# Kernel optimization log

Hardware: AMD Instinct MI355X
Metric: run time of the kernel (lower is better)

The kernel has to match this reference:

```python
import jax, jax.numpy as jnp
import numpy as np

RATIO = 4


def setup_inputs() -> dict:
    key = jax.random.key(0)
    ks = jax.random.split(key, 6)
    b, c, hw = 8, 64, 256
    n = (hw // RATIO) ** 2  # 4096
    return {
        "x": jax.random.normal(ks[0], (b, c, hw, hw), dtype=jnp.float32),
        "weight": jax.random.normal(ks[1], (n, n), dtype=jnp.float32) * 0.01,
        "pih_w": jax.random.normal(ks[2], (c, c, 3, 3), dtype=jnp.float32) * 0.05,
        "pih_b": jax.random.normal(ks[3], (c,), dtype=jnp.float32) * 0.05,
        "up_w": jax.random.normal(ks[4], (c, c, 4, 4), dtype=jnp.float32) * 0.05,
        "up_b": jax.random.normal(ks[5], (c,), dtype=jnp.float32) * 0.05,
    }


def reference(x, weight, pih_w, pih_b, up_w, up_b):
    b, c, h, w = x.shape
    identity = x
    # MaxPool2d(ratio)
    xp = jax.lax.reduce_window(x, -jnp.inf, jax.lax.max,
                               (1, 1, RATIO, RATIO), (1, 1, RATIO, RATIO), 'VALID')
    # 3x3 conv, pad 1
    x_pih = jax.lax.conv_general_dilated(
        xp, pih_w, window_strides=(1, 1), padding='SAME',
        dimension_numbers=('NCHW', 'OIHW', 'NCHW')) + pih_b[None, :, None, None]
    x_pih = jax.nn.relu(x_pih).reshape(b, c, -1)  # [b, c, N]
    # F.normalize(p=2, dim=2)
    nrm = jnp.sqrt(jnp.sum(x_pih * x_pih, axis=2, keepdims=True))
    nx = x_pih / jnp.maximum(nrm, 1e-12)
    # channel-channel affinity [b, c, c]
    A = jnp.einsum('bcn,bdn->bcd', nx, nx)
    # vectorized D^{-1/2}, replacing per-batch torch.diag loop
    d = 1.0 / jnp.sqrt(jnp.sum(A, axis=2) + 1e-8)  # [b, c]
    d = jnp.where(jnp.isfinite(d), d, 0.0)
    L = jnp.eye(c, dtype=x.dtype)[None] - d[:, :, None] * A * d[:, None, :]
    # diffusion: L @ x_flat @ W
    xf = xp.reshape(b, c, -1)  # [b, c, N]
    out = jnp.einsum('bcd,bdn->bcn', L, xf)
    out = jnp.einsum('bcn,nm->bcm', out, weight)
    hp, wp = h // RATIO, w // RATIO
    out = out.reshape(b, c, hp, wp)
    # ConvTranspose2d(k=4, s=4): each pixel expands to a 4x4 block
    up = jnp.einsum('bchw,coij->bohiwj', out, up_w).reshape(b, c, h, w)
    up = up + up_b[None, :, None, None]
    return jax.nn.relu(up + identity)
```

## Files before the change

kernel.cpp:

```cpp
#include <hip/hip_runtime.h>

#define NB 8
#define NC 64
#define HW 256
#define HP 64
#define NN 4096

typedef unsigned short u16;
typedef unsigned int u32;
typedef __attribute__((ext_vector_type(8))) short s16x8;
typedef __attribute__((ext_vector_type(8))) unsigned short u16x8;
typedef __attribute__((ext_vector_type(4))) unsigned short u16x4;
typedef __attribute__((ext_vector_type(4))) float f32x4;

__device__ __forceinline__ u16 f2bf(float f) {
    unsigned u = __float_as_uint(f);
    return (u16)((u + 0x7fffu + ((u >> 16) & 1u)) >> 16);
}
__device__ __forceinline__ float bf2f(u16 v) {
    return __uint_as_float(((unsigned)v) << 16);
}

#define GLOAD16(gsrc, ldst) \
    __builtin_amdgcn_global_load_lds((const __attribute__((address_space(1))) unsigned int*)(gsrc), \
                                     (__attribute__((address_space(3))) unsigned int*)(ldst), 16, 0, 0)

__global__ __launch_bounds__(256) void maxpool_nhwc_k(const float* __restrict__ x,
                                                      u16* __restrict__ xpc) {
    __shared__ u16 tile[64 * 66];
    int bid = blockIdx.x;
    int b = bid >> 6, y = bid & 63;
    int t = threadIdx.x;
    int cl  = t >> 3;
    int seg = t & 7;
#pragma unroll
    for (int pass = 0; pass < 2; ++pass) {
        int c = pass * 32 + cl;
        const float* p = x + ((long)(b * 64 + c) * 256 + y * 4) * 256 + seg * 32;
        float m[8];
#pragma unroll
        for (int i = 0; i < 8; ++i) m[i] = -3.4e38f;
#pragma unroll
        for (int r = 0; r < 4; ++r)
#pragma unroll
            for (int i = 0; i < 8; ++i) {
                float4 v = *(const float4*)(p + r * 256 + i * 4);
                m[i] = fmaxf(m[i], fmaxf(fmaxf(v.x, v.y), fmaxf(v.z, v.w)));
            }
#pragma unroll
        for (int i = 0; i < 8; ++i) tile[c * 66 + seg * 8 + i] = f2bf(m[i]);
    }
    __syncthreads();
    int xo = t >> 2, cp = t & 3;
    u16x8 o0, o1;
#pragma unroll
    for (int e = 0; e < 8; ++e) o0[e] = tile[(cp * 16 + e) * 66 + xo];
#pragma unroll
    for (int e = 0; e < 8; ++e) o1[e] = tile[(cp * 16 + 8 + e) * 66 + xo];
    u16* dst = xpc + ((long)(b * 4096 + y * 64 + xo)) * 64 + cp * 16;
    *(u16x8*)dst = o0;
    *(u16x8*)(dst + 8) = o1;
}

__global__ __launch_bounds__(256) void transW_k(const float* __restrict__ W,
                                                u16* __restrict__ WTb) {
    __shared__ alignas(16) u16 tile[128 * 128];
    int k0 = (blockIdx.x >> 5) * 128;
    int n0 = (blockIdx.x & 31) * 128;
    int t = threadIdx.x;
    int nq = t & 31;
#pragma unroll
    for (int p = 0; p < 4; ++p) {
        int kq = (t >> 5) + p * 8;
        float4 v[4];
#pragma unroll
        for (int j = 0; j < 4; ++j)
            v[j] = *(const float4*)&W[(long)(k0 + kq * 4 + j) * 4096 + n0 + nq * 4];
#pragma unroll
        for (int jn = 0; jn < 4; ++jn) {
            int n = nq * 4 + jn;
            u16x4 c4;
            c4[0] = f2bf(((const float*)&v[0])[jn]);
            c4[1] = f2bf(((const float*)&v[1])[jn]);
            c4[2] = f2bf(((const float*)&v[2])[jn]);
            c4[3] = f2bf(((const float*)&v[3])[jn]);
            *(u16x4*)((char*)tile + n * 256 + ((kq * 8) ^ ((n & 15) << 4))) = c4;
        }
    }
    __syncthreads();
#pragma unroll
    for (int q = 0; q < 8; ++q) {
        int chunk = t + q * 256;
        int n = chunk >> 4, seg = chunk & 15;
        u16x8 o = *(const u16x8*)((const char*)tile + n * 256 +
                                  ((seg * 16) ^ ((n & 15) << 4)));
        *(u16x8*)&WTb[(long)(n0 + n) * 4096 + k0 + seg * 8] = o;
    }
}

__global__ __launch_bounds__(256) void prep_k(const float* __restrict__ uw,
                                              const float* __restrict__ pw,
                                              u16* __restrict__ Wb,
                                              u16* __restrict__ Bpack) {
    int bid = blockIdx.x;
    int t = threadIdx.x;
    if (bid < 256) {
        int idx = bid * 256 + t;
        int c = idx & 63;
        int n = idx >> 6;
        int o = n >> 4, i = (n >> 2) & 3, j = n & 3;
        Wb[idx] = f2bf(uw[((c * 64 + o) * 4 + i) * 4 + j]);
    } else {
        int idx = (bid - 256) * 256 + t;
        if (idx >= 36864) return;
        int e = idx & 7, l = (idx >> 3) & 63, nf = (idx >> 9) & 3, s = idx >> 11;
        int ch = s & 1, kd = s >> 1;
        int dy = kd / 3, dx = kd % 3;
        int o  = nf * 16 + (l & 15);
        int ci = ch * 32 + (l >> 4) * 8 + e;
        Bpack[idx] = f2bf(pw[((o * 64 + ci) * 3 + dy) * 3 + dx]);
    }
}

__global__ __launch_bounds__(256) void convgram_k(const u16* __restrict__ xpc,
                                                  const u16* __restrict__ Bpack,
                                                  const float* __restrict__ pb,
                                                  float* __restrict__ G) {
    __shared__ alignas(16) u16 ldsIn[3 * 66 * 64];
    __shared__ alignas(16) u16 ldsX[64 * 64];
    int bid = blockIdx.x;
    int b = bid >> 6, y = bid & 63;
    int t = threadIdx.x;
    int w = t >> 6, l = t & 63;
    int lr = l & 15, ksub = l >> 4;

    if (t < 48) {
        int r = t >> 4, q = t & 15;
        int off = r * 8448 + (q < 8 ? q * 16 : 8320 + (q - 8) * 16);
        *(u16x8*)((char*)ldsIn + off) = (u16x8){0, 0, 0, 0, 0, 0, 0, 0};
    }
#pragma unroll
    for (int i = 0; i < 6; ++i) {
        int r  = i >> 1;
        int ya = y - 1 + r;
        int wro = (i & 1) * 4096 + t * 16;
        int dst = r * 8448 + 128 + wro;
        if (ya >= 0 && ya < 64) {
            int xsl = 1 + (wro >> 7);
            int srcoff = (wro & ~127) | ((wro & 127) ^ ((xsl & 7) << 4));
            GLOAD16((const char*)xpc + (long)(b * 64 + ya) * 8192 + srcoff,
                    (char*)ldsIn + dst);
        } else {
            *(u16x8*)((char*)ldsIn + dst) = (u16x8){0, 0, 0, 0, 0, 0, 0, 0};
        }
    }
    __syncthreads();

    f32x4 acc[4];
#pragma unroll
    for (int mf = 0; mf < 4; ++mf) acc[mf] = (f32x4){0.f, 0.f, 0.f, 0.f};

#pragma unroll
    for (int kd = 0; kd < 9; ++kd) {
        int dy = kd / 3, dx = kd % 3;
#pragma unroll
        for (int ch = 0; ch < 2; ++ch) {
            int s = kd * 2 + ch;
            s16x8 bfrag = *(const s16x8*)(Bpack + ((s * 4 + w) * 64 + l) * 8);
#pragma unroll
            for (int mf = 0; mf < 4; ++mf) {
                int xsl  = mf * 16 + lr + dx;
                int coff = (ch * 64 + ksub * 16) ^ ((xsl & 7) << 4);
                s16x8 af = *(const s16x8*)((const char*)ldsIn +
                                           dy * 8448 + xsl * 128 + coff);
                acc[mf] = __builtin_amdgcn_mfma_f32_16x16x32_bf16(
                    af, bfrag, acc[mf], 0, 0, 0);
            }
        }
    }
    int o = w * 16 + lr;
    float bias = pb[o];
#pragma unroll
    for (int mf = 0; mf < 4; ++mf)
#pragma unroll
        for (int rp = 0; rp < 2; ++rp) {
            u16 lo = f2bf(fmaxf(acc[mf][rp * 2]     + bias, 0.f));
            u16 hi = f2bf(fmaxf(acc[mf][rp * 2 + 1] + bias, 0.f));
            int nb   = (mf * 16 + ksub * 4 + rp * 2) * 2;
            int boff = nb ^ ((o & 7) << 4);
            *(u32*)((char*)ldsX + o * 128 + boff) = (u32)lo | ((u32)hi << 16);
        }
    __syncthreads();

    f32x4 g[4];
#pragma unroll
    for (int nf = 0; nf < 4; ++nf) g[nf] = (f32x4){0.f, 0.f, 0.f, 0.f};
#pragma unroll
    for (int kk = 0; kk < 2; ++kk) {
        int kb = kk * 64 + ksub * 16;
        int arow = w * 16 + lr;
        s16x8 af = *(const s16x8*)((const char*)ldsX + arow * 128 +
                                   (kb ^ ((arow & 7) << 4)));
#pragma unroll
        for (int nf = 0; nf < 4; ++nf) {
            int brow = nf * 16 + lr;
            s16x8 bf = *(const s16x8*)((const char*)ldsX + brow * 128 +
                                       (kb ^ ((brow & 7) << 4)));
            g[nf] = __builtin_amdgcn_mfma_f32_16x16x32_bf16(af, bf, g[nf], 0, 0, 0);
        }
    }
    float* Gb = G + b * 4096;
#pragma unroll
    for (int nf = 0; nf < 4; ++nf)
#pragma unroll
        for (int r = 0; r < 4; ++r)
            atomicAdd(&Gb[(w * 16 + ksub * 4 + r) * 64 + nf * 16 + lr], g[nf][r]);
}

__global__ __launch_bounds__(256) void diffuse_mfma_k(const float* __restrict__ G,
                                                      const u16* __restrict__ xpc,
                                                      u16* __restrict__ Ab16) {
    __shared__ alignas(16) u16 lds[128 * 64];
    __shared__ alignas(16) u16 ldsL[64 * 64];
    __shared__ float nrm[64], dvv[64];
    int n0 = blockIdx.x * 128;
    int b  = blockIdx.y;
    int t = threadIdx.x;
    int w = t >> 6, l = t & 63;
    int lr = l & 15, ksub = l >> 4;

#pragma unroll
    for (int i = 0; i < 4; ++i) {
        int d = i * 4096 + t * 16;
        int row = d >> 7, off = d & 127;
        GLOAD16((const char*)xpc + ((long)(b * 4096 + n0 + row)) * 128 +
                (off ^ ((row & 7) << 4)),
                (char*)lds + d);
    }

    const float* Gb = G + b * 4096;
    if (t < 64) nrm[t] = fmaxf(sqrtf(Gb[t * 64 + t]), 1e-12f);
    __syncthreads();
    if (t < 64) {
        float nc = nrm[t];
        float rs = 0.f;
        for (int d = 0; d < 64; ++d) rs += Gb[t * 64 + d] / (nc * nrm[d]);
        float dd = 1.0f / sqrtf(rs + 1e-8f);
        if (!(dd <= 3.0e38f)) dd = 0.0f;
        dvv[t] = dd;
    }
    __syncthreads();
    {
        int c = t >> 2;
        int dbase = (t & 3) * 16;
        float nc = nrm[c], dc = dvv[c];
#pragma unroll
        for (int dp2 = 0; dp2 < 8; ++dp2) {
            int d0 = dbase + dp2 * 2;
            float A0 = Gb[c * 64 + d0]     / (nc * nrm[d0]);
            float A1 = Gb[c * 64 + d0 + 1] / (nc * nrm[d0 + 1]);
            float v0 = ((c == d0)     ? 1.f : 0.f) - dc * A0 * dvv[d0];
            float v1 = ((c == d0 + 1) ? 1.f : 0.f) - dc * A1 * dvv[d0 + 1];
            int o = c * 64 + (d0 ^ ((c & 7) << 3));
            *(u32*)&ldsL[o] = (u32)f2bf(v0) | ((u32)f2bf(v1) << 16);
        }
    }
    __syncthreads();

    f32x4 acc[4][2];
#pragma unroll
    for (int mf = 0; mf < 4; ++mf)
#pragma unroll
        for (int nq = 0; nq < 2; ++nq) acc[mf][nq] = (f32x4){0.f, 0.f, 0.f, 0.f};

#pragma unroll
    for (int kk = 0; kk < 2; ++kk) {
        s16x8 bfr[2];
#pragma unroll
        for (int nq = 0; nq < 2; ++nq) {
            int brow = w * 32 + nq * 16 + lr;
            bfr[nq] = *(const s16x8*)((const char*)lds + brow * 128 +
                                      ((kk * 64 + ksub * 16) ^ ((brow & 7) << 4)));
        }
#pragma unroll
        for (int mf = 0; mf < 4; ++mf) {
            int arow = mf * 16 + lr;
            s16x8 af = *(const s16x8*)((const char*)ldsL + arow * 128 +
                                       ((kk * 64 + ksub * 16) ^ ((arow & 7) << 4)));
#pragma unroll
            for (int nq = 0; nq < 2; ++nq)
                acc[mf][nq] = __builtin_amdgcn_mfma_f32_16x16x32_bf16(
                    af, bfr[nq], acc[mf][nq], 0, 0, 0);
        }
    }
#pragma unroll
    for (int mf = 0; mf < 4; ++mf)
#pragma unroll
        for (int nq = 0; nq < 2; ++nq)
#pragma unroll
            for (int r = 0; r < 4; ++r)
                Ab16[((long)(b * 64 + mf * 16 + (l >> 4) * 4 + r)) * 4096 +
                     n0 + w * 32 + nq * 16 + lr] = f2bf(acc[mf][nq][r]);
}

#define KSPLIT 4
#define KSLICE 1024
__global__ __launch_bounds__(256) void gemm_mfma_k(const u16* __restrict__ A,
                                                   const u16* __restrict__ WT,
                                                   u16* __restrict__ Cp) {
    __shared__ alignas(16) u16 ldsA[8192];
    __shared__ alignas(16) u16 ldsB[8192];
    int bid = blockIdx.x;
    int swz = (bid & 7) * 64 + (bid >> 3);
    int m0 = (swz & 3) * 128;
    int n0 = ((swz >> 2) & 31) * 128;
    int z  = swz >> 7;
    int t = threadIdx.x;
    int w = t >> 6, l = t & 63;
    int wr = w >> 1, wc = w & 1;
    int lr = l & 15;
    int lk = (l >> 4) << 4;

    f32x4 acc[4][4];
#pragma unroll
    for (int mf = 0; mf < 4; ++mf)
#pragma unroll
        for (int nf = 0; nf < 4; ++nf) acc[mf][nf] = (f32x4){0.f, 0.f, 0.f, 0.f};

    const char* Ab = (const char*)(A  + (long)m0 * 4096 + z * KSLICE);
    const char* Bb = (const char*)(WT + (long)n0 * 4096 + z * KSLICE);

    for (int k0 = 0; k0 < KSLICE; k0 += 64) {
        __syncthreads();
#pragma unroll
        for (int i = 0; i < 4; ++i) {
            int d   = i * 4096 + t * 16;
            int row = d >> 7;
            int off = d & 127;
            int sk  = off ^ ((row & 7) << 4);
            GLOAD16(Ab + (long)row * 8192 + k0 * 2 + sk, (char*)ldsA + d);
            GLOAD16(Bb + (long)row * 8192 + k0 * 2 + sk, (char*)ldsB + d);
        }
        __syncthreads();
#pragma unroll
        for (int kk = 0; kk < 2; ++kk) {
            s16x8 af[4], bf[4];
#pragma unroll
            for (int f = 0; f < 4; ++f) {
                int ar = wr * 64 + f * 16 + lr;
                af[f] = *(const s16x8*)((const char*)ldsA + ar * 128 +
                                        ((kk * 64 + lk) ^ ((ar & 7) << 4)));
                int br = wc * 64 + f * 16 + lr;
                bf[f] = *(const s16x8*)((const char*)ldsB + br * 128 +
                                        ((kk * 64 + lk) ^ ((br & 7) << 4)));
            }
#pragma unroll
            for (int mf = 0; mf < 4; ++mf)
#pragma unroll
                for (int nf = 0; nf < 4; ++nf)
                    acc[mf][nf] = __builtin_amdgcn_mfma_f32_16x16x32_bf16(
                        af[mf], bf[nf], acc[mf][nf], 0, 0, 0);
        }
    }
    int tile = (swz & 3) * 32 + ((swz >> 2) & 31);
    u16 carr[64];
#pragma unroll
    for (int mf = 0; mf < 4; ++mf)
#pragma unroll
        for (int nf = 0; nf < 4; ++nf)
#pragma unroll
            for (int r = 0; r < 4; ++r)
                carr[mf * 16 + nf * 4 + r] = f2bf(acc[mf][nf][r]);
    u16* dp = Cp + ((long)(z * 128 + tile) * 256 + t) * 64;
#pragma unroll
    for (int v8 = 0; v8 < 8; ++v8)
        *(u16x8*)&dp[v8 * 8] = *(const u16x8*)&carr[v8 * 8];
}

__global__ __launch_bounds__(256) void convT_mfma_k(const u16* __restrict__ Cp,
                                                    const u16* __restrict__ Wb,
                                                    const float* __restrict__ ub,
                                                    const float* __restrict__ x,
                                                    float* __restrict__ out) {
    __shared__ alignas(16) char smem[34816];
    u16*   ldsA = (u16*)smem;
    u16*   ldsB = (u16*)(smem + 16384);
    float* ldsC = (float*)smem;
    int bid = blockIdx.x;
    int swzb = (bid & 7) * 256 + (bid >> 3);
    int mt = swzb >> 3;
    int nt = swzb & 7;
    int m0 = mt * 128;
    int n0 = nt * 128;
    int t = threadIdx.x;
    int w = t >> 6, l = t & 63;
    int wr = w >> 1, wc = w & 1;
    int lr = l & 15;
    int lkb = (l >> 4) << 4;

    const char* Bb = (const char*)(Wb + (long)n0 * 64);
#pragma unroll
    for (int i = 0; i < 4; ++i) {
        int d = i * 4096 + t * 16;
        int srcoff = (d & ~127) | ((d & 127) ^ (((d >> 7) & 7) << 4));
        GLOAD16(Bb + srcoff, (char*)ldsB + d);
    }

    {
        int b_   = mt >> 5;
        int wr_g = b_ & 1;
        int tile_g = (b_ >> 1) * 32 + (mt & 31);
        int tg = wr_g * 128 + (t & 127);
        int h  = t >> 7;
        int l_g = tg & 63, wc_g = (tg >> 6) & 1;
        int k4 = l_g >> 4, lr_g = l_g & 15;
        float s[32];
#pragma unroll
        for (int k = 0; k < 32; ++k) s[k] = 0.f;
        const u16* dpb = Cp + ((long)tile_g * 256 + tg) * 64 + h * 32;
#pragma unroll
        for (int z = 0; z < KSPLIT; ++z) {
            const u16* pz = dpb + (long)z * 2097152;
#pragma unroll
            for (int j = 0; j < 4; ++j) {
                u16x8 vv = *(const u16x8*)&pz[j * 8];
#pragma unroll
                for (int e = 0; e < 8; ++e) s[j * 8 + e] += bf2f(vv[e]);
            }
        }
#pragma unroll
        for (int j = 0; j < 4; ++j) {
            int v8 = h * 4 + j;
            int mf = v8 >> 1;
            int c0 = mf * 16 + k4 * 4;
#pragma unroll
            for (int q = 0; q < 2; ++q) {
                int nf  = (v8 & 1) * 2 + q;
                int pix = wc_g * 64 + nf * 16 + lr_g;
                int sw  = (pix & 7) << 4;
                int f   = j * 8 + q * 4;
                u32 w0 = (u32)f2bf(s[f + 0]) | ((u32)f2bf(s[f + 1]) << 16);
                u32 w1 = (u32)f2bf(s[f + 2]) | ((u32)f2bf(s[f + 3]) << 16);
                *(u32*)((char*)ldsA + pix * 128 + ((c0 * 2) ^ sw))     = w0;
                *(u32*)((char*)ldsA + pix * 128 + ((c0 * 2 + 4) ^ sw)) = w1;
            }
        }
    }
    __syncthreads();

    f32x4 acc[4][4];
#pragma unroll
    for (int mf = 0; mf < 4; ++mf)
#pragma unroll
        for (int nf = 0; nf < 4; ++nf) acc[mf][nf] = (f32x4){0.f, 0.f, 0.f, 0.f};

#pragma unroll
    for (int kk = 0; kk < 2; ++kk) {
        s16x8 af[4], bfg[4];
#pragma unroll
        for (int f = 0; f < 4; ++f) {
            int ar = wr * 64 + f * 16 + lr;
            af[f] = *(const s16x8*)((const char*)ldsA + ar * 128 +
                                    ((kk * 64 + lkb) ^ ((ar & 7) << 4)));
            int br = wc * 64 + f * 16 + lr;
            bfg[f] = *(const s16x8*)((const char*)ldsB + br * 128 +
                                     ((kk * 64 + lkb) ^ ((br & 7) << 4)));
        }
#pragma unroll
        for (int mf = 0; mf < 4; ++mf)
#pragma unroll
            for (int nf = 0; nf < 4; ++nf)
                acc[mf][nf] = __builtin_amdgcn_mfma_f32_16x16x32_bf16(
                    af[mf], bfg[nf], acc[mf][nf], 0, 0, 0);
    }
    __syncthreads();

#pragma unroll
    for (int nh = 0; nh < 2; ++nh) {
        if (nh) __syncthreads();
        if (wc == nh) {
#pragma unroll
            for (int mf = 0; mf < 4; ++mf)
#pragma unroll
                for (int nf = 0; nf < 4; ++nf)
#pragma unroll
                    for (int r = 0; r < 4; ++r) {
                        int row = wr * 64 + mf * 16 + (l >> 4) * 4 + r;
                        int col = nf * 16 + lr;
                        ldsC[row * 68 + (col ^ (((row >> 3) & 7) << 2))] =
                            acc[mf][nf][r];
                    }
        }
        __syncthreads();
#pragma unroll
        for (int q = 0; q < 2; ++q) {
            int idx = q * 256 + t;
            int ml = idx & 127;
            int oo = idx >> 7;
            int o  = nt * 8 + nh * 4 + oo;
            float bias = ub[o];
            int mg = m0 + ml;
            int b = mg >> 12, pix = mg & 4095;
            int h2 = pix >> 6, ww = pix & 63;
            long base = ((long)(b * 64 + o) * 256 + h2 * 4) * 256 + ww * 4;
#pragma unroll
            for (int i = 0; i < 4; ++i) {
                f32x4 cv = *(const f32x4*)&ldsC[ml * 68 +
                            ((oo * 16 + i * 4) ^ (((ml >> 3) & 7) << 2))];
                float4 xi = *(const float4*)&x[base + i * 256];
                float4 rr;
                rr.x = fmaxf(cv[0] + bias + xi.x, 0.f);
                rr.y = fmaxf(cv[1] + bias + xi.y, 0.f);
                rr.z = fmaxf(cv[2] + bias + xi.z, 0.f);
                rr.w = fmaxf(cv[3] + bias + xi.w, 0.f);
                *(float4*)&out[base + i * 256] = rr;
            }
        }
    }
}

extern "C" void kernel_launch(void* const* d_in, const int* in_sizes, int n_in,
                              void* d_out, int out_size, void* d_ws, size_t ws_size,
                              hipStream_t stream) {
    const float* x      = (const float*)d_in[0];
    const float* weight = (const float*)d_in[1];
    const float* pih_w  = (const float*)d_in[2];
    const float* pih_b  = (const float*)d_in[3];
    const float* up_w   = (const float*)d_in[4];
    const float* up_b   = (const float*)d_in[5];
    float* out = (float*)d_out;
    float* ws  = (float*)d_ws;

    u16*   xpc   = (u16*)ws;
    u16*   Ab16  = (u16*)(ws + 3145728);
    float* G     = ws + 4194304;
    u16*   Wb    = (u16*)(ws + 4259840);
    u16*   WTb   = (u16*)(ws + 4325376);
    u16*   Cp    = (u16*)(ws + 12713984);
    u16*   Bpack = Cp + 2097152;

    hipMemsetAsync(G, 0, 32768 * sizeof(float), stream);
    maxpool_nhwc_k<<<512, 256, 0, stream>>>(x, xpc);
    transW_k      <<<1024, 256, 0, stream>>>(weight, WTb);
    prep_k        <<<400, 256, 0, stream>>>(up_w, pih_w, Wb, Bpack);
    convgram_k    <<<512, 256, 0, stream>>>(xpc, Bpack, pih_b, G);
    diffuse_mfma_k<<<dim3(32, 8), 256, 0, stream>>>(G, xpc, Ab16);
    gemm_mfma_k   <<<512, 256, 0, stream>>>(Ab16, WTb, Cp);
    convT_mfma_k  <<<2048, 256, 0, stream>>>(Cp, Wb, up_b, x, out);
}
```

Before: 163.2 us.

## Drop split-K in big GEMM, write transposed output directly; merge front prep kernels

The 512x4096x4096 GEMM moves from a 128x128 tile with 4-way split-K, which wrote bf16 partials and made the convT kernel sum them, to a 64x64 tile over the full K range. The output goes through LDS and is stored transposed in the pixel-major layout convT expects, so convT can load its A operand directly with global_load_lds. Separately, the maxpool, weight-transpose and param-prep kernels are merged into one launch. This removes the partial-sum traffic and two launches. The cost is smaller tiles with less operand reuse (each wave does 2x2 MFMAs per k-step) and a longer serial K loop per block.

```diff
diff --git a/kernel.cpp b/kernel.cpp
--- a/kernel.cpp
+++ b/kernel.cpp
@@ -25,100 +25,100 @@
     __builtin_amdgcn_global_load_lds((const __attribute__((address_space(1))) unsigned int*)(gsrc), \
                                      (__attribute__((address_space(3))) unsigned int*)(ldst), 16, 0, 0)
 
-__global__ __launch_bounds__(256) void maxpool_nhwc_k(const float* __restrict__ x,
-                                                      u16* __restrict__ xpc) {
-    __shared__ u16 tile[64 * 66];
-    int bid = blockIdx.x;
-    int b = bid >> 6, y = bid & 63;
-    int t = threadIdx.x;
-    int cl  = t >> 3;
-    int seg = t & 7;
-#pragma unroll
-    for (int pass = 0; pass < 2; ++pass) {
-        int c = pass * 32 + cl;
-        const float* p = x + ((long)(b * 64 + c) * 256 + y * 4) * 256 + seg * 32;
-        float m[8];
-#pragma unroll
-        for (int i = 0; i < 8; ++i) m[i] = -3.4e38f;
-#pragma unroll
-        for (int r = 0; r < 4; ++r)
-#pragma unroll
-            for (int i = 0; i < 8; ++i) {
-                float4 v = *(const float4*)(p + r * 256 + i * 4);
-                m[i] = fmaxf(m[i], fmaxf(fmaxf(v.x, v.y), fmaxf(v.z, v.w)));
-            }
-#pragma unroll
-        for (int i = 0; i < 8; ++i) tile[c * 66 + seg * 8 + i] = f2bf(m[i]);
-    }
-    __syncthreads();
-    int xo = t >> 2, cp = t & 3;
-    u16x8 o0, o1;
-#pragma unroll
-    for (int e = 0; e < 8; ++e) o0[e] = tile[(cp * 16 + e) * 66 + xo];
-#pragma unroll
-    for (int e = 0; e < 8; ++e) o1[e] = tile[(cp * 16 + 8 + e) * 66 + xo];
-    u16* dst = xpc + ((long)(b * 4096 + y * 64 + xo)) * 64 + cp * 16;
-    *(u16x8*)dst = o0;
-    *(u16x8*)(dst + 8) = o1;
-}
-
-__global__ __launch_bounds__(256) void transW_k(const float* __restrict__ W,
-                                                u16* __restrict__ WTb) {
-    __shared__ alignas(16) u16 tile[128 * 128];
-    int k0 = (blockIdx.x >> 5) * 128;
-    int n0 = (blockIdx.x & 31) * 128;
-    int t = threadIdx.x;
-    int nq = t & 31;
-#pragma unroll
-    for (int p = 0; p < 4; ++p) {
-        int kq = (t >> 5) + p * 8;
-        float4 v[4];
-#pragma unroll
-        for (int j = 0; j < 4; ++j)
-            v[j] = *(const float4*)&W[(long)(k0 + kq * 4 + j) * 4096 + n0 + nq * 4];
-#pragma unroll
-        for (int jn = 0; jn < 4; ++jn) {
-            int n = nq * 4 + jn;
-            u16x4 c4;
-            c4[0] = f2bf(((const float*)&v[0])[jn]);
-            c4[1] = f2bf(((const float*)&v[1])[jn]);
-            c4[2] = f2bf(((const float*)&v[2])[jn]);
-            c4[3] = f2bf(((const float*)&v[3])[jn]);
-            *(u16x4*)((char*)tile + n * 256 + ((kq * 8) ^ ((n & 15) << 4))) = c4;
-        }
-    }
-    __syncthreads();
-#pragma unroll
-    for (int q = 0; q < 8; ++q) {
-        int chunk = t + q * 256;
-        int n = chunk >> 4, seg = chunk & 15;
-        u16x8 o = *(const u16x8*)((const char*)tile + n * 256 +
-                                  ((seg * 16) ^ ((n & 15) << 4)));
-        *(u16x8*)&WTb[(long)(n0 + n) * 4096 + k0 + seg * 8] = o;
-    }
-}
-
-__global__ __launch_bounds__(256) void prep_k(const float* __restrict__ uw,
-                                              const float* __restrict__ pw,
-                                              u16* __restrict__ Wb,
-                                              u16* __restrict__ Bpack) {
+__global__ __launch_bounds__(256) void front_k(const float* __restrict__ x,
+                                               const float* __restrict__ W,
+                                               const float* __restrict__ uw,
+                                               const float* __restrict__ pw,
+                                               u16* __restrict__ xpc,
+                                               u16* __restrict__ WTb,
+                                               u16* __restrict__ Wb,
+                                               u16* __restrict__ Bpack) {
+    __shared__ alignas(16) char sm[32768];
     int bid = blockIdx.x;
     int t = threadIdx.x;
-    if (bid < 256) {
-        int idx = bid * 256 + t;
-        int c = idx & 63;
-        int n = idx >> 6;
-        int o = n >> 4, i = (n >> 2) & 3, j = n & 3;
-        Wb[idx] = f2bf(uw[((c * 64 + o) * 4 + i) * 4 + j]);
+    if (bid < 512) {
+        u16* tile = (u16*)sm;
+        int b = bid >> 6, y = bid & 63;
+        int cl  = t >> 3;
+        int seg = t & 7;
+#pragma unroll
+        for (int pass = 0; pass < 2; ++pass) {
+            int c = pass * 32 + cl;
+            const float* p = x + ((long)(b * 64 + c) * 256 + y * 4) * 256 + seg * 32;
+            float m[8];
+#pragma unroll
+            for (int i = 0; i < 8; ++i) m[i] = -3.4e38f;
+#pragma unroll
+            for (int r = 0; r < 4; ++r)
+#pragma unroll
+                for (int i = 0; i < 8; ++i) {
+                    float4 v = *(const float4*)(p + r * 256 + i * 4);
+                    m[i] = fmaxf(m[i], fmaxf(fmaxf(v.x, v.y), fmaxf(v.z, v.w)));
+                }
+#pragma unroll
+            for (int i = 0; i < 8; ++i) tile[c * 66 + seg * 8 + i] = f2bf(m[i]);
+        }
+        __syncthreads();
+        int xo = t >> 2, cp = t & 3;
+        u16x8 o0, o1;
+#pragma unroll
+        for (int e = 0; e < 8; ++e) o0[e] = tile[(cp * 16 + e) * 66 + xo];
+#pragma unroll
+        for (int e = 0; e < 8; ++e) o1[e] = tile[(cp * 16 + 8 + e) * 66 + xo];
+        u16* dst = xpc + ((long)(b * 4096 + y * 64 + xo)) * 64 + cp * 16;
+        *(u16x8*)dst = o0;
+        *(u16x8*)(dst + 8) = o1;
+    } else if (bid < 1536) {
+        u16* tile = (u16*)sm;
+        int tb = bid - 512;
+        int k0 = (tb >> 5) * 128;
+        int n0 = (tb & 31) * 128;
+        int nq = t & 31;
+#pragma unroll
+        for (int p = 0; p < 4; ++p) {
+            int kq = (t >> 5) + p * 8;
+            float4 v[4];
+#pragma unroll
+            for (int j = 0; j < 4; ++j)
+                v[j] = *(const float4*)&W[(long)(k0 + kq * 4 + j) * 4096 + n0 + nq * 4];
+#pragma unroll
+            for (int jn = 0; jn < 4; ++jn) {
+                int n = nq * 4 + jn;
+                u16x4 c4;
+                c4[0] = f2bf(((const float*)&v[0])[jn]);
+                c4[1] = f2bf(((const float*)&v[1])[jn]);
+                c4[2] = f2bf(((const float*)&v[2])[jn]);
+                c4[3] = f2bf(((const float*)&v[3])[jn]);
+                *(u16x4*)((char*)tile + n * 256 + ((kq * 8) ^ ((n & 15) << 4))) = c4;
+            }
+        }
+        __syncthreads();
+#pragma unroll
+        for (int q = 0; q < 8; ++q) {
+            int chunk = t + q * 256;
+            int n = chunk >> 4, seg = chunk & 15;
+            u16x8 o = *(const u16x8*)((const char*)tile + n * 256 +
+                                      ((seg * 16) ^ ((n & 15) << 4)));
+            *(u16x8*)&WTb[(long)(n0 + n) * 4096 + k0 + seg * 8] = o;
+        }
     } else {
-        int idx = (bid - 256) * 256 + t;
-        if (idx >= 36864) return;
-        int e = idx & 7, l = (idx >> 3) & 63, nf = (idx >> 9) & 3, s = idx >> 11;
-        int ch = s & 1, kd = s >> 1;
-        int dy = kd / 3, dx = kd % 3;
-        int o  = nf * 16 + (l & 15);
-        int ci = ch * 32 + (l >> 4) * 8 + e;
-        Bpack[idx] = f2bf(pw[((o * 64 + ci) * 3 + dy) * 3 + dx]);
+        int pbid = bid - 1536;
+        if (pbid < 256) {
+            int idx = pbid * 256 + t;
+            int c = idx & 63;
+            int n = idx >> 6;
+            int o = n >> 4, i = (n >> 2) & 3, j = n & 3;
+            Wb[idx] = f2bf(uw[((c * 64 + o) * 4 + i) * 4 + j]);
+        } else {
+            int idx = (pbid - 256) * 256 + t;
+            if (idx >= 36864) return;
+            int e = idx & 7, l = (idx >> 3) & 63, nf = (idx >> 9) & 3, s = idx >> 11;
+            int ch = s & 1, kd = s >> 1;
+            int dy = kd / 3, dx = kd % 3;
+            int o  = nf * 16 + (l & 15);
+            int ci = ch * 32 + (l >> 4) * 8 + e;
+            Bpack[idx] = f2bf(pw[((o * 64 + ci) * 3 + dy) * 3 + dx]);
+        }
     }
 }
 
@@ -303,37 +303,36 @@
                      n0 + w * 32 + nq * 16 + lr] = f2bf(acc[mf][nq][r]);
 }
 
-#define KSPLIT 4
-#define KSLICE 1024
 __global__ __launch_bounds__(256) void gemm_mfma_k(const u16* __restrict__ A,
                                                    const u16* __restrict__ WT,
-                                                   u16* __restrict__ Cp) {
-    __shared__ alignas(16) u16 ldsA[8192];
-    __shared__ alignas(16) u16 ldsB[8192];
+                                                   u16* __restrict__ A2) {
+    __shared__ alignas(16) char smem[16384];
+    u16* ldsA = (u16*)smem;
+    u16* ldsB = (u16*)(smem + 8192);
+    float* ldsC = (float*)smem;
     int bid = blockIdx.x;
-    int swz = (bid & 7) * 64 + (bid >> 3);
-    int m0 = (swz & 3) * 128;
-    int n0 = ((swz >> 2) & 31) * 128;
-    int z  = swz >> 7;
+    int b   = bid & 7;
+    int n0p = (bid >> 3) * 64;
+    int m0  = b * 64;
     int t = threadIdx.x;
     int w = t >> 6, l = t & 63;
     int wr = w >> 1, wc = w & 1;
     int lr = l & 15;
     int lk = (l >> 4) << 4;
 
-    f32x4 acc[4][4];
-#pragma unroll
-    for (int mf = 0; mf < 4; ++mf)
-#pragma unroll
-        for (int nf = 0; nf < 4; ++nf) acc[mf][nf] = (f32x4){0.f, 0.f, 0.f, 0.f};
-
-    const char* Ab = (const char*)(A  + (long)m0 * 4096 + z * KSLICE);
-    const char* Bb = (const char*)(WT + (long)n0 * 4096 + z * KSLICE);
-
-    for (int k0 = 0; k0 < KSLICE; k0 += 64) {
+    f32x4 acc[2][2];
+#pragma unroll
+    for (int mf = 0; mf < 2; ++mf)
+#pragma unroll
+        for (int nf = 0; nf < 2; ++nf) acc[mf][nf] = (f32x4){0.f, 0.f, 0.f, 0.f};
+
+    const char* Ab = (const char*)(A  + (long)m0 * 4096);
+    const char* Bb = (const char*)(WT + (long)n0p * 4096);
+
+    for (int k0 = 0; k0 < 4096; k0 += 64) {
         __syncthreads();
 #pragma unroll
-        for (int i = 0; i < 4; ++i) {
+        for (int i = 0; i < 2; ++i) {
             int d   = i * 4096 + t * 16;
             int row = d >> 7;
             int off = d & 127;
@@ -344,40 +343,52 @@
         __syncthreads();
 #pragma unroll
         for (int kk = 0; kk < 2; ++kk) {
-            s16x8 af[4], bf[4];
-#pragma unroll
-            for (int f = 0; f < 4; ++f) {
-                int ar = wr * 64 + f * 16 + lr;
+            s16x8 af[2], bf[2];
+#pragma unroll
+            for (int f = 0; f < 2; ++f) {
+                int ar = wr * 32 + f * 16 + lr;
                 af[f] = *(const s16x8*)((const char*)ldsA + ar * 128 +
                                         ((kk * 64 + lk) ^ ((ar & 7) << 4)));
-                int br = wc * 64 + f * 16 + lr;
+                int br = wc * 32 + f * 16 + lr;
                 bf[f] = *(const s16x8*)((const char*)ldsB + br * 128 +
                                         ((kk * 64 + lk) ^ ((br & 7) << 4)));
             }
 #pragma unroll
-            for (int mf = 0; mf < 4; ++mf)
-#pragma unroll
-                for (int nf = 0; nf < 4; ++nf)
+            for (int mf = 0; mf < 2; ++mf)
+#pragma unroll
+                for (int nf = 0; nf < 2; ++nf)
                     acc[mf][nf] = __builtin_amdgcn_mfma_f32_16x16x32_bf16(
                         af[mf], bf[nf], acc[mf][nf], 0, 0, 0);
         }
     }
-    int tile = (swz & 3) * 32 + ((swz >> 2) & 31);
-    u16 carr[64];
-#pragma unroll
-    for (int mf = 0; mf < 4; ++mf)
-#pragma unroll
-        for (int nf = 0; nf < 4; ++nf)
-#pragma unroll
-            for (int r = 0; r < 4; ++r)
-                carr[mf * 16 + nf * 4 + r] = f2bf(acc[mf][nf][r]);
-    u16* dp = Cp + ((long)(z * 128 + tile) * 256 + t) * 64;
-#pragma unroll
-    for (int v8 = 0; v8 < 8; ++v8)
-        *(u16x8*)&dp[v8 * 8] = *(const u16x8*)&carr[v8 * 8];
-}
-
-__global__ __launch_bounds__(256) void convT_mfma_k(const u16* __restrict__ Cp,
+    __syncthreads();
+#pragma unroll
+    for (int mf = 0; mf < 2; ++mf)
+#pragma unroll
+        for (int nf = 0; nf < 2; ++nf)
+#pragma unroll
+            for (int r = 0; r < 4; ++r) {
+                int c = wr * 32 + mf * 16 + (l >> 4) * 4 + r;
+                int p = wc * 32 + nf * 16 + lr;
+                ldsC[p * 64 + (c ^ ((p & 7) << 2))] = acc[mf][nf][r];
+            }
+    __syncthreads();
+    {
+        int p = t >> 2, c0 = (t & 3) * 16;
+        u16 vals[16];
+#pragma unroll
+        for (int a = 0; a < 4; ++a) {
+            f32x4 v = *(const f32x4*)&ldsC[p * 64 + ((c0 + a * 4) ^ ((p & 7) << 2))];
+#pragma unroll
+            for (int j = 0; j < 4; ++j) vals[a * 4 + j] = f2bf(v[j]);
+        }
+        u16* dst = A2 + ((long)(b * 4096 + n0p + p)) * 64 + c0;
+        *(u16x8*)dst       = *(const u16x8*)&vals[0];
+        *(u16x8*)(dst + 8) = *(const u16x8*)&vals[8];
+    }
+}
+
+__global__ __launch_bounds__(256) void convT_mfma_k(const u16* __restrict__ A2,
                                                     const u16* __restrict__ Wb,
                                                     const float* __restrict__ ub,
                                                     const float* __restrict__ x,
@@ -398,53 +409,14 @@
     int lr = l & 15;
     int lkb = (l >> 4) << 4;
 
+    const char* Ab = (const char*)(A2 + (long)m0 * 64);
     const char* Bb = (const char*)(Wb + (long)n0 * 64);
 #pragma unroll
     for (int i = 0; i < 4; ++i) {
         int d = i * 4096 + t * 16;
         int srcoff = (d & ~127) | ((d & 127) ^ (((d >> 7) & 7) << 4));
+        GLOAD16(Ab + srcoff, (char*)ldsA + d);
         GLOAD16(Bb + srcoff, (char*)ldsB + d);
-    }
-
-    {
-        int b_   = mt >> 5;
-        int wr_g = b_ & 1;
-        int tile_g = (b_ >> 1) * 32 + (mt & 31);
-        int tg = wr_g * 128 + (t & 127);
-        int h  = t >> 7;
-        int l_g = tg & 63, wc_g = (tg >> 6) & 1;
-        int k4 = l_g >> 4, lr_g = l_g & 15;
-        float s[32];
-#pragma unroll
-        for (int k = 0; k < 32; ++k) s[k] = 0.f;
-        const u16* dpb = Cp + ((long)tile_g * 256 + tg) * 64 + h * 32;
-#pragma unroll
-        for (int z = 0; z < KSPLIT; ++z) {
-            const u16* pz = dpb + (long)z * 2097152;
-#pragma unroll
-            for (int j = 0; j < 4; ++j) {
-                u16x8 vv = *(const u16x8*)&pz[j * 8];
-#pragma unroll
-                for (int e = 0; e < 8; ++e) s[j * 8 + e] += bf2f(vv[e]);
-            }
-        }
-#pragma unroll
-        for (int j = 0; j < 4; ++j) {
-            int v8 = h * 4 + j;
-            int mf = v8 >> 1;
-            int c0 = mf * 16 + k4 * 4;
-#pragma unroll
-            for (int q = 0; q < 2; ++q) {
-                int nf  = (v8 & 1) * 2 + q;
-                int pix = wc_g * 64 + nf * 16 + lr_g;
-                int sw  = (pix & 7) << 4;
-                int f   = j * 8 + q * 4;
-                u32 w0 = (u32)f2bf(s[f + 0]) | ((u32)f2bf(s[f + 1]) << 16);
-                u32 w1 = (u32)f2bf(s[f + 2]) | ((u32)f2bf(s[f + 3]) << 16);
-                *(u32*)((char*)ldsA + pix * 128 + ((c0 * 2) ^ sw))     = w0;
-                *(u32*)((char*)ldsA + pix * 128 + ((c0 * 2 + 4) ^ sw)) = w1;
-            }
-        }
     }
     __syncthreads();
 
@@ -536,15 +508,14 @@
     float* G     = ws + 4194304;
     u16*   Wb    = (u16*)(ws + 4259840);
     u16*   WTb   = (u16*)(ws + 4325376);
-    u16*   Cp    = (u16*)(ws + 12713984);
-    u16*   Bpack = Cp + 2097152;
+    u16*   A2    = (u16*)(ws + 12713984);
+    u16*   Bpack = A2 + 2097152;
 
     hipMemsetAsync(G, 0, 32768 * sizeof(float), stream);
-    maxpool_nhwc_k<<<512, 256, 0, stream>>>(x, xpc);
-    transW_k      <<<1024, 256, 0, stream>>>(weight, WTb);
-    prep_k        <<<400, 256, 0, stream>>>(up_w, pih_w, Wb, Bpack);
+    front_k       <<<1936, 256, 0, stream>>>(x, weight, up_w, pih_w,
+                                             xpc, WTb, Wb, Bpack);
     convgram_k    <<<512, 256, 0, stream>>>(xpc, Bpack, pih_b, G);
     diffuse_mfma_k<<<dim3(32, 8), 256, 0, stream>>>(G, xpc, Ab16);
-    gemm_mfma_k   <<<512, 256, 0, stream>>>(Ab16, WTb, Cp);
-    convT_mfma_k  <<<2048, 256, 0, stream>>>(Cp, Wb, up_b, x, out);
-}
+    gemm_mfma_k   <<<512, 256, 0, stream>>>(Ab16, WTb, A2);
+    convT_mfma_k  <<<2048, 256, 0, stream>>>(A2, Wb, up_b, x, out);
+}
```

Result: no change. 163.4 us (+0.1%).
